# Kernel optimization log

Hardware: AMD Instinct MI355X
Metric: run time of the kernel (lower is better)

Reference implementation:

```python
import jax, jax.numpy as jnp
import numpy as np

SEQ_LEN, BATCH, INPUT, HIDDEN = 2048, 128, 256, 512

def _xavier(key, shape):
    fan_out, fan_in = shape
    limit = float(np.sqrt(6.0 / (fan_in + fan_out)))
    return jax.random.uniform(key, shape, jnp.float32, -limit, limit)

def setup_inputs() -> dict:
    key = jax.random.key(0)
    ks = jax.random.split(key, 9)
    return {
        "x_seq": jax.random.normal(ks[0], (SEQ_LEN, BATCH, INPUT), jnp.float32),
        "h": jnp.zeros((BATCH, HIDDEN), jnp.float32),
        "U_c": _xavier(ks[1], (HIDDEN, INPUT)),
        "w_c": jax.random.normal(ks[2], (HIDDEN,), jnp.float32),
        "b_c": jax.random.normal(ks[3], (HIDDEN,), jnp.float32),
        "U_a": _xavier(ks[4], (HIDDEN, INPUT)),
        "w_a": jax.random.normal(ks[5], (HIDDEN,), jnp.float32),
        "b_a": jax.random.normal(ks[6], (HIDDEN,), jnp.float32),
        "U_h": _xavier(ks[7], (HIDDEN, INPUT)),
    }

def reference(x_seq, h, U_c, w_c, b_c, U_a, w_a, b_a, U_h):
    # Precompute all input projections in three batched GEMMs: (S,B,I)@(I,H)->(S,B,H)
    xc = jnp.einsum("sbi,hi->sbh", x_seq, U_c) + b_c
    xa = jnp.einsum("sbi,hi->sbh", x_seq, U_a) + b_a
    xh = jnp.einsum("sbi,hi->sbh", x_seq, U_h)

    def step(h, inputs):
        xc_t, xa_t, xh_t = inputs
        c = jax.nn.sigmoid(xc_t + w_c * h)
        a = 1.0 + jnp.tanh(xa_t + w_a * h)
        h_new = c * h + (1.0 - c) * jnp.tanh(xh_t + a * h)
        return h_new, h_new

    hn, output = jax.lax.scan(step, h, (xc, xa, xh))
    return output, hn
```

## Files before the change

### kernel.cpp

```cpp
#include <hip/hip_runtime.h>
#include <hip/hip_bf16.h>


typedef _Float16 half8 __attribute__((ext_vector_type(8)));
typedef float    f32x4 __attribute__((ext_vector_type(4)));

#define SEQ   2048
#define BATCH 128
#define INP   256
#define HID   512
#define CHUNK_T 256
#define NCHUNK  8
#define MLOC  (CHUNK_T * BATCH)
#define BJ    (BATCH * HID)

__global__ __launch_bounds__(256) void cvt_split(
    const float* __restrict__ src, _Float16* __restrict__ hi,
    _Float16* __restrict__ lo, int n8)
{
    int i = blockIdx.x * blockDim.x + threadIdx.x;
    int stride = gridDim.x * blockDim.x;
    for (; i < n8; i += stride) {
        f32x4 a = ((const f32x4*)src)[2 * i];
        f32x4 b = ((const f32x4*)src)[2 * i + 1];
        half8 h, l;
#pragma unroll
        for (int k = 0; k < 4; ++k) {
            _Float16 hh = (_Float16)a[k];
            h[k] = hh; l[k] = (_Float16)(a[k] - (float)hh);
        }
#pragma unroll
        for (int k = 0; k < 4; ++k) {
            _Float16 hh = (_Float16)b[k];
            h[4 + k] = hh; l[4 + k] = (_Float16)(b[k] - (float)hh);
        }
        ((half8*)hi)[i] = h;
        ((half8*)lo)[i] = l;
    }
}

__device__ __forceinline__ void llds16(const void* g, void* l)
{
    __builtin_amdgcn_global_load_lds(
        (const __attribute__((address_space(1))) unsigned int*)g,
        (__attribute__((address_space(3))) unsigned int*)l,
        16, 0, 0);
}

__global__ __launch_bounds__(256) void gemm_xu(
    const _Float16* __restrict__ Ah, const _Float16* __restrict__ Al,
    const _Float16* __restrict__ Bh, const _Float16* __restrict__ Bl,
    float* __restrict__ C)
{
    __shared__ __align__(16) _Float16 AsH[8192];
    __shared__ __align__(16) _Float16 AsL[8192];
    __shared__ __align__(16) _Float16 BsH[8192];
    __shared__ __align__(16) _Float16 BsL[8192];

    const int tid  = threadIdx.x;
    const int lane = tid & 63;
    const int wv   = tid >> 6;
    const int quad = lane >> 4;
    const int l16  = lane & 15;
    const int m0   = blockIdx.x * 128;
    const int n0   = blockIdx.y * 128;
    const int wm   = (wv >> 1) * 64;
    const int wn   = (wv & 1) * 64;

    f32x4 acc[4][4];
    const f32x4 zero = {0.0f, 0.0f, 0.0f, 0.0f};
#pragma unroll
    for (int i = 0; i < 4; ++i)
#pragma unroll
        for (int j = 0; j < 4; ++j) acc[i][j] = zero;

    for (int ko = 0; ko < 4; ++ko) {
        const int k0 = ko * 64;
        __syncthreads();
#pragma unroll
        for (int i = 0; i < 4; ++i) {
            const int s  = i * 256 + tid;
            const int r  = s >> 3;
            const int cg = (s & 7) ^ (r & 7);
            const size_t ga = (size_t)(m0 + r) * INP + k0 + cg * 8;
            const size_t gb = (size_t)(n0 + r) * INP + k0 + cg * 8;
            const size_t dst = (size_t)(i * 256 + wv * 64) * 16;
            llds16(Ah + ga, (char*)AsH + dst);
            llds16(Al + ga, (char*)AsL + dst);
            llds16(Bh + gb, (char*)BsH + dst);
            llds16(Bl + gb, (char*)BsL + dst);
        }
        __syncthreads();
#pragma unroll
        for (int ks = 0; ks < 2; ++ks) {
            const int cgk = ks * 4 + quad;
            half8 ah[4], al[4], bh[4], bl[4];
#pragma unroll
            for (int mf = 0; mf < 4; ++mf) {
                const int row = wm + mf * 16 + l16;
                const size_t off = (size_t)(row * 8 + (cgk ^ (row & 7))) * 8;
                ah[mf] = *(const half8*)(AsH + off);
                al[mf] = *(const half8*)(AsL + off);
            }
#pragma unroll
            for (int nf = 0; nf < 4; ++nf) {
                const int row = wn + nf * 16 + l16;
                const size_t off = (size_t)(row * 8 + (cgk ^ (row & 7))) * 8;
                bh[nf] = *(const half8*)(BsH + off);
                bl[nf] = *(const half8*)(BsL + off);
            }
#pragma unroll
            for (int mf = 0; mf < 4; ++mf)
#pragma unroll
                for (int nf = 0; nf < 4; ++nf) {
                    acc[mf][nf] = __builtin_amdgcn_mfma_f32_16x16x32_f16(
                        ah[mf], bh[nf], acc[mf][nf], 0, 0, 0);
                    acc[mf][nf] = __builtin_amdgcn_mfma_f32_16x16x32_f16(
                        ah[mf], bl[nf], acc[mf][nf], 0, 0, 0);
                    acc[mf][nf] = __builtin_amdgcn_mfma_f32_16x16x32_f16(
                        al[mf], bh[nf], acc[mf][nf], 0, 0, 0);
                }
        }
    }

    const int g   = n0 >> 9;
    const int nIn = n0 & 511;
#pragma unroll
    for (int mf = 0; mf < 4; ++mf)
#pragma unroll
        for (int nf = 0; nf < 4; ++nf)
#pragma unroll
            for (int r = 0; r < 4; ++r) {
                const int m = m0 + wm + mf * 16 + quad * 4 + r;
                const int j = nIn + wn + nf * 16 + l16;
                C[(size_t)m * 1536 + (size_t)j * 3 + g] = acc[mf][nf][r];
            }
}

__device__ __forceinline__ float tanh_acc(float z)
{
    return 1.0f - 2.0f / (expf(2.0f * z) + 1.0f);
}

__global__ __launch_bounds__(256) void brc_scan(
    const float* __restrict__ X,
    const float* __restrict__ h_in, float* __restrict__ h_out,
    const float* __restrict__ wc, const float* __restrict__ bc,
    const float* __restrict__ wa, const float* __restrict__ ba,
    float* __restrict__ out)
{
    const int bj = blockIdx.x * 256 + threadIdx.x;
    const int j  = bj & (HID - 1);
    float h = h_in[bj];
    const float wcj = wc[j], bcj = bc[j];
    const float waj = wa[j], baj = ba[j];

    size_t idx = (size_t)bj * 3;
    float nxc = X[idx], nxa = X[idx + 1], nxh = X[idx + 2];
    const size_t step = (size_t)BJ * 3;

    for (int t = 0; t < CHUNK_T; ++t) {
        const float xc = nxc, xa = nxa, xh = nxh;
        idx += step;
        if (t + 1 < CHUNK_T) {
            nxc = X[idx]; nxa = X[idx + 1]; nxh = X[idx + 2];
        }
        const float c  = 1.0f / (1.0f + expf(-(xc + bcj + wcj * h)));
        const float a  = 1.0f + tanh_acc(xa + baj + waj * h);
        const float th = tanh_acc(xh + a * h);
        h = c * h + (1.0f - c) * th;
        out[(size_t)t * BJ + bj] = h;
    }
    h_out[bj] = h;
}

extern "C" void kernel_launch(void* const* d_in, const int* in_sizes, int n_in,
                              void* d_out, int out_size, void* d_ws, size_t ws_size,
                              hipStream_t stream)
{
    const float* x  = (const float*)d_in[0];
    const float* h0 = (const float*)d_in[1];
    const float* Uc = (const float*)d_in[2];
    const float* wc = (const float*)d_in[3];
    const float* bc = (const float*)d_in[4];
    const float* Ua = (const float*)d_in[5];
    const float* wa = (const float*)d_in[6];
    const float* ba = (const float*)d_in[7];
    const float* Uh = (const float*)d_in[8];
    float* out = (float*)d_out;

    char* ws = (char*)d_ws;
    const size_t XCH = (size_t)MLOC * INP;
    _Float16* xhi = (_Float16*)ws;
    _Float16* xlo = xhi + XCH;
    _Float16* Uhi = xlo + XCH;
    _Float16* Ulo = Uhi + (size_t)3 * HID * INP;
    float* chunkBuf = (float*)(Ulo + (size_t)3 * HID * INP);
    float* hstate = chunkBuf + (size_t)MLOC * 1536;

    cvt_split<<<64, 256, 0, stream>>>(Uc, Uhi,                 Ulo,                 HID * INP / 8);
    cvt_split<<<64, 256, 0, stream>>>(Ua, Uhi + HID * INP,     Ulo + HID * INP,     HID * INP / 8);
    cvt_split<<<64, 256, 0, stream>>>(Uh, Uhi + 2 * HID * INP, Ulo + 2 * HID * INP, HID * INP / 8);

    for (int chunk = 0; chunk < NCHUNK; ++chunk) {
        const float* xc = x + (size_t)chunk * MLOC * INP;
        cvt_split<<<4096, 256, 0, stream>>>(xc, xhi, xlo, MLOC * INP / 8);

        gemm_xu<<<dim3(256, 12), 256, 0, stream>>>(xhi, xlo, Uhi, Ulo, chunkBuf);

        const float* hin = (chunk == 0) ? h0 : hstate;
        float* hout = (chunk == NCHUNK - 1) ? (out + (size_t)SEQ * BJ) : hstate;
        brc_scan<<<256, 256, 0, stream>>>(
            chunkBuf, hin, hout, wc, bc, wa, ba,
            out + (size_t)chunk * CHUNK_T * BJ);
    }
}
```

Before: 2.928 ms.

## Software-pipeline scan, GEMM and conversion of successive chunks in one fused launch

Merges the conversion, GEMM and scan kernels into one launch. Block ranges are split by role, and each launch works on a different chunk: it scans chunk k, runs the GEMM for chunk k+1 and converts chunk k+2, with the staging buffers double-buffered. The goal is to overlap the latency-bound, low-occupancy scan (256 blocks) with the compute-heavy GEMM instead of running them back to back. The scan also gets a deeper 4-step prefetch of X and nontemporal output stores. The cost is double the workspace, and every block reserves the GEMM's 64KB of shared memory, which may limit how many blocks can be resident alongside the scan blocks.

```diff
diff --git a/kernel.cpp b/kernel.cpp
--- a/kernel.cpp
+++ b/kernel.cpp
@@ -14,12 +14,15 @@
 #define MLOC  (CHUNK_T * BATCH)
 #define BJ    (BATCH * HID)
 
-__global__ __launch_bounds__(256) void cvt_split(
+#define NS_BLK 256
+#define NG_BLK 3072
+#define NC_BLK 512
+#define TOT_BLK (NS_BLK + NG_BLK + NC_BLK)
+
+__device__ __forceinline__ void cvt_body(
     const float* __restrict__ src, _Float16* __restrict__ hi,
-    _Float16* __restrict__ lo, int n8)
-{
-    int i = blockIdx.x * blockDim.x + threadIdx.x;
-    int stride = gridDim.x * blockDim.x;
+    _Float16* __restrict__ lo, int n8, int i, int stride)
+{
     for (; i < n8; i += stride) {
         f32x4 a = ((const f32x4*)src)[2 * i];
         f32x4 b = ((const f32x4*)src)[2 * i + 1];
@@ -39,6 +42,14 @@
     }
 }
 
+__global__ __launch_bounds__(256) void cvt_split(
+    const float* __restrict__ src, _Float16* __restrict__ hi,
+    _Float16* __restrict__ lo, int n8)
+{
+    cvt_body(src, hi, lo, n8,
+             blockIdx.x * blockDim.x + threadIdx.x, gridDim.x * blockDim.x);
+}
+
 __device__ __forceinline__ void llds16(const void* g, void* l)
 {
     __builtin_amdgcn_global_load_lds(
@@ -47,23 +58,19 @@
         16, 0, 0);
 }
 
-__global__ __launch_bounds__(256) void gemm_xu(
+__device__ __forceinline__ void gemm_body(int bid,
     const _Float16* __restrict__ Ah, const _Float16* __restrict__ Al,
     const _Float16* __restrict__ Bh, const _Float16* __restrict__ Bl,
-    float* __restrict__ C)
-{
-    __shared__ __align__(16) _Float16 AsH[8192];
-    __shared__ __align__(16) _Float16 AsL[8192];
-    __shared__ __align__(16) _Float16 BsH[8192];
-    __shared__ __align__(16) _Float16 BsL[8192];
-
+    float* __restrict__ C,
+    _Float16* AsH, _Float16* AsL, _Float16* BsH, _Float16* BsL)
+{
     const int tid  = threadIdx.x;
     const int lane = tid & 63;
     const int wv   = tid >> 6;
     const int quad = lane >> 4;
     const int l16  = lane & 15;
-    const int m0   = blockIdx.x * 128;
-    const int n0   = blockIdx.y * 128;
+    const int m0   = (bid & 255) * 128;
+    const int n0   = (bid >> 8) * 128;
     const int wm   = (wv >> 1) * 64;
     const int wn   = (wv & 1) * 64;
 
@@ -142,36 +149,77 @@
     return 1.0f - 2.0f / (expf(2.0f * z) + 1.0f);
 }
 
-__global__ __launch_bounds__(256) void brc_scan(
+__device__ __forceinline__ void scan_body(int bid,
     const float* __restrict__ X,
     const float* __restrict__ h_in, float* __restrict__ h_out,
     const float* __restrict__ wc, const float* __restrict__ bc,
     const float* __restrict__ wa, const float* __restrict__ ba,
     float* __restrict__ out)
 {
-    const int bj = blockIdx.x * 256 + threadIdx.x;
+    const int bj = bid * 256 + threadIdx.x;
     const int j  = bj & (HID - 1);
     float h = h_in[bj];
     const float wcj = wc[j], bcj = bc[j];
     const float waj = wa[j], baj = ba[j];
 
     size_t idx = (size_t)bj * 3;
-    float nxc = X[idx], nxa = X[idx + 1], nxh = X[idx + 2];
     const size_t step = (size_t)BJ * 3;
 
+    float px[4][3];
+#pragma unroll
+    for (int i = 0; i < 4; ++i) {
+        px[i][0] = X[idx]; px[i][1] = X[idx + 1]; px[i][2] = X[idx + 2];
+        idx += step;
+    }
+#pragma unroll 4
     for (int t = 0; t < CHUNK_T; ++t) {
-        const float xc = nxc, xa = nxa, xh = nxh;
-        idx += step;
-        if (t + 1 < CHUNK_T) {
-            nxc = X[idx]; nxa = X[idx + 1]; nxh = X[idx + 2];
+        const int s = t & 3;
+        const float xc = px[s][0], xa = px[s][1], xh = px[s][2];
+        if (t + 4 < CHUNK_T) {
+            px[s][0] = X[idx]; px[s][1] = X[idx + 1]; px[s][2] = X[idx + 2];
+            idx += step;
         }
         const float c  = 1.0f / (1.0f + expf(-(xc + bcj + wcj * h)));
         const float a  = 1.0f + tanh_acc(xa + baj + waj * h);
         const float th = tanh_acc(xh + a * h);
         h = c * h + (1.0f - c) * th;
-        out[(size_t)t * BJ + bj] = h;
+        __builtin_nontemporal_store(h, &out[(size_t)t * BJ + bj]);
     }
     h_out[bj] = h;
+}
+
+__global__ __launch_bounds__(256) void fused_step(
+    const float* __restrict__ scanX, const float* __restrict__ h_in,
+    float* __restrict__ h_out, float* __restrict__ scanOut,
+    const float* __restrict__ wc, const float* __restrict__ bc,
+    const float* __restrict__ wa, const float* __restrict__ ba,
+    const _Float16* __restrict__ gAh, const _Float16* __restrict__ gAl,
+    const _Float16* __restrict__ gBh, const _Float16* __restrict__ gBl,
+    float* __restrict__ gC,
+    const float* __restrict__ cvtSrc, _Float16* __restrict__ cvtHi,
+    _Float16* __restrict__ cvtLo)
+{
+    __shared__ __align__(16) _Float16 AsH[8192];
+    __shared__ __align__(16) _Float16 AsL[8192];
+    __shared__ __align__(16) _Float16 BsH[8192];
+    __shared__ __align__(16) _Float16 BsL[8192];
+
+    int bid = blockIdx.x;
+    if (bid < NS_BLK) {
+        if (scanX)
+            scan_body(bid, scanX, h_in, h_out, wc, bc, wa, ba, scanOut);
+        return;
+    }
+    bid -= NS_BLK;
+    if (bid < NG_BLK) {
+        if (gAh)
+            gemm_body(bid, gAh, gAl, gBh, gBl, gC, AsH, AsL, BsH, BsL);
+        return;
+    }
+    bid -= NG_BLK;
+    if (cvtSrc)
+        cvt_body(cvtSrc, cvtHi, cvtLo, MLOC * INP / 8,
+                 bid * 256 + (int)threadIdx.x, NC_BLK * 256);
 }
 
 extern "C" void kernel_launch(void* const* d_in, const int* in_sizes, int n_in,
@@ -191,27 +239,49 @@
 
     char* ws = (char*)d_ws;
     const size_t XCH = (size_t)MLOC * INP;
-    _Float16* xhi = (_Float16*)ws;
-    _Float16* xlo = xhi + XCH;
-    _Float16* Uhi = xlo + XCH;
+    _Float16* xhiB[2]; _Float16* xloB[2];
+    xhiB[0] = (_Float16*)ws;
+    xloB[0] = xhiB[0] + XCH;
+    xhiB[1] = xloB[0] + XCH;
+    xloB[1] = xhiB[1] + XCH;
+    _Float16* Uhi = xloB[1] + XCH;
     _Float16* Ulo = Uhi + (size_t)3 * HID * INP;
-    float* chunkBuf = (float*)(Ulo + (size_t)3 * HID * INP);
-    float* hstate = chunkBuf + (size_t)MLOC * 1536;
+    float* bufB[2];
+    bufB[0] = (float*)(Ulo + (size_t)3 * HID * INP);
+    bufB[1] = bufB[0] + (size_t)MLOC * 1536;
+    float* hstate = bufB[1] + (size_t)MLOC * 1536;
 
     cvt_split<<<64, 256, 0, stream>>>(Uc, Uhi,                 Ulo,                 HID * INP / 8);
     cvt_split<<<64, 256, 0, stream>>>(Ua, Uhi + HID * INP,     Ulo + HID * INP,     HID * INP / 8);
     cvt_split<<<64, 256, 0, stream>>>(Uh, Uhi + 2 * HID * INP, Ulo + 2 * HID * INP, HID * INP / 8);
-
-    for (int chunk = 0; chunk < NCHUNK; ++chunk) {
-        const float* xc = x + (size_t)chunk * MLOC * INP;
-        cvt_split<<<4096, 256, 0, stream>>>(xc, xhi, xlo, MLOC * INP / 8);
-
-        gemm_xu<<<dim3(256, 12), 256, 0, stream>>>(xhi, xlo, Uhi, Ulo, chunkBuf);
-
-        const float* hin = (chunk == 0) ? h0 : hstate;
-        float* hout = (chunk == NCHUNK - 1) ? (out + (size_t)SEQ * BJ) : hstate;
-        brc_scan<<<256, 256, 0, stream>>>(
-            chunkBuf, hin, hout, wc, bc, wa, ba,
-            out + (size_t)chunk * CHUNK_T * BJ);
-    }
-}
+    cvt_split<<<4096, 256, 0, stream>>>(x, xhiB[0], xloB[0], MLOC * INP / 8);
+
+    for (int k = -1; k < NCHUNK; ++k) {
+        const int kg = k + 1, kc = k + 2;
+
+        const float* scanX = nullptr; const float* hin = nullptr;
+        float* hout = nullptr; float* sout = nullptr;
+        if (k >= 0) {
+            scanX = bufB[k & 1];
+            hin   = (k == 0) ? h0 : hstate;
+            hout  = (k == NCHUNK - 1) ? (out + (size_t)SEQ * BJ) : hstate;
+            sout  = out + (size_t)k * CHUNK_T * BJ;
+        }
+
+        const _Float16* gah = nullptr; const _Float16* gal = nullptr;
+        float* gc = nullptr;
+        if (kg < NCHUNK) {
+            gah = xhiB[kg & 1]; gal = xloB[kg & 1]; gc = bufB[kg & 1];
+        }
+
+        const float* csrc = nullptr; _Float16* chi = nullptr; _Float16* clo = nullptr;
+        if (kc < NCHUNK) {
+            csrc = x + (size_t)kc * MLOC * INP;
+            chi = xhiB[kc & 1]; clo = xloB[kc & 1];
+        }
+
+        fused_step<<<TOT_BLK, 256, 0, stream>>>(
+            scanX, hin, hout, sout, wc, bc, wa, ba,
+            gah, gal, Uhi, Ulo, gc, csrc, chi, clo);
+    }
+}
```

Measured after the change: 3.289 ms. +12.3%, slower.
